# Kernel optimization log

Measured on AMD Instinct MI355X. Metric: run time of the kernel, lower is better.

## Reference

```python
import jax, jax.numpy as jnp
import numpy as np

N_NODES = 50000
N_GRAPHS = 64
HEADS = 4
OUT_CH = 32
HC = HEADS * OUT_CH  # 128
F_IN = 32
EDGE_DIM = 1
NEG_SLOPE = 0.2


def gat_conv(x, edge_index, W, att_src, att_dst, bias, edge_attr=None, W_edge=None, att_edge=None):
    """PyG GATConv (concat=True, add_self_loops=True, fill_value='mean', eval mode)."""
    N = x.shape[0]
    H, C = att_src.shape
    xs = (x @ W).reshape(N, H, C)                      # [N,H,C]
    a_src = (xs * att_src).sum(-1)                     # [N,H]
    a_dst = (xs * att_dst).sum(-1)                     # [N,H]

    src, dst = edge_index[0], edge_index[1]
    loops = jnp.arange(N)
    src_sl = jnp.concatenate([src, loops])
    dst_sl = jnp.concatenate([dst, loops])

    alpha = a_src[src_sl] + a_dst[dst_sl]              # [E+N,H]
    if edge_attr is not None:
        # self-loop edge_attr = per-dst mean of incoming edge_attr (fill_value='mean')
        cnt = jax.ops.segment_sum(jnp.ones_like(dst, dtype=edge_attr.dtype), dst, N)
        loop_attr = jax.ops.segment_sum(edge_attr, dst, N) / jnp.maximum(cnt, 1.0)[:, None]
        ea = jnp.concatenate([edge_attr, loop_attr], axis=0)
        e = (ea @ W_edge).reshape(-1, H, C)
        alpha = alpha + (e * att_edge).sum(-1)

    alpha = jax.nn.leaky_relu(alpha, NEG_SLOPE)
    # segment softmax over incoming edges of each dst node
    amax = jax.ops.segment_max(alpha, dst_sl, N)       # every node has a self loop
    alpha = jnp.exp(alpha - amax[dst_sl])
    denom = jax.ops.segment_sum(alpha, dst_sl, N)
    alpha = alpha / (denom[dst_sl] + 1e-16)

    msg = xs[src_sl] * alpha[:, :, None]               # [E+N,H,C]
    out = jax.ops.segment_sum(msg, dst_sl, N)          # [N,H,C]
    return out.reshape(N, H * C) + bias


def setup_inputs() -> dict:
    key = jax.random.key(0)
    ks = iter(jax.random.split(key, 40))
    d = {}
    d["x"] = jax.random.normal(next(ks), (N_NODES, F_IN), jnp.float32)
    d["covalent_index"] = jax.random.randint(next(ks), (2, 150000), 0, N_NODES)
    d["distance_index"] = jax.random.randint(next(ks), (2, 1600000), 0, N_NODES)
    d["distance_attr"] = jax.random.uniform(next(ks), (1600000, EDGE_DIM), jnp.float32)
    d["batch"] = jnp.sort(jax.random.randint(next(ks), (N_NODES,), 0, N_GRAPHS))

    def p(shape):
        return jax.random.normal(next(ks), shape, jnp.float32) * 0.1

    for name, fin in [("c1", F_IN), ("c2", HC), ("d1", F_IN), ("d2", HC)]:
        d[f"W_{name}"] = p((fin, HC))
        d[f"as_{name}"] = p((HEADS, OUT_CH))
        d[f"ad_{name}"] = p((HEADS, OUT_CH))
        d[f"b_{name}"] = p((HC,))
    for name in ("d1", "d2"):
        d[f"We_{name}"] = p((EDGE_DIM, HC))
        d[f"ae_{name}"] = p((HEADS, OUT_CH))
    d["ff_W"] = p((HC, 128))
    d["ff_b"] = p((128,))
    d["out_W"] = p((128, 1))
    d["out_b"] = p((1,))
    return d


def reference(x, covalent_index, distance_index, distance_attr, batch,
              W_c1, as_c1, ad_c1, b_c1, W_c2, as_c2, ad_c2, b_c2,
              W_d1, as_d1, ad_d1, b_d1, We_d1, ae_d1,
              W_d2, as_d2, ad_d2, b_d2, We_d2, ae_d2,
              ff_W, ff_b, out_W, out_b):
    # covalent branch
    x1 = gat_conv(x, covalent_index, W_c1, as_c1, ad_c1, b_c1)
    x1 = jax.nn.relu(x1)
    x1 = gat_conv(x1, covalent_index, W_c2, as_c2, ad_c2, b_c2)
    # distance branch (with edge attributes)
    x2 = gat_conv(x, distance_index, W_d1, as_d1, ad_d1, b_d1, distance_attr, We_d1, ae_d1)
    x2 = jax.nn.relu(x2)
    x2 = gat_conv(x2, distance_index, W_d2, as_d2, ad_d2, b_d2, distance_attr, We_d2, ae_d2)
    h = (x1 + x2) * 0.5
    # global mean pool per graph
    sums = jax.ops.segment_sum(h, batch, N_GRAPHS)
    cnts = jax.ops.segment_sum(jnp.ones((h.shape[0],), h.dtype), batch, N_GRAPHS)
    g = sums / jnp.maximum(cnts, 1.0)[:, None]
    g = jax.nn.relu(g @ ff_W + ff_b)
    # dropout(p=0.3) treated as identity (eval / deterministic reference)
    return jax.nn.sigmoid(g @ out_W + out_b)
```

## Files before the change

### kernel.cpp

```cpp
#include <hip/hip_runtime.h>
#include <math.h>

#define NEG_SLOPE 0.2f

__device__ __forceinline__ float lrelu(float x){ return x > 0.f ? x : NEG_SLOPE * x; }
__device__ __forceinline__ float bf_lo(unsigned u){ return __uint_as_float(u << 16); }
__device__ __forceinline__ float bf_hi(unsigned u){ return __uint_as_float(u & 0xffff0000u); }
__device__ __forceinline__ unsigned short f2bf(float v){
  unsigned ub = __float_as_uint(v);
  return (unsigned short)((ub + 0x7FFFu + ((ub >> 16) & 1u)) >> 16);
}

template<int K>
__global__ __launch_bounds__(256) void transform2_kernel(
    const float* __restrict__ A, const float* __restrict__ W,
    const float* __restrict__ att_s, const float* __restrict__ att_d,
    unsigned short* __restrict__ xs, float* __restrict__ a_src,
    float* __restrict__ a_dst, int N){
  constexpr int KC = (K < 32) ? K : 32;
  __shared__ float sW[KC][128];
  __shared__ float sA[32][K];
  const int tid = threadIdx.x;
  const int j4  = (tid & 31) * 4;
  const int ng  = tid >> 5;
  const int h   = (tid & 31) >> 3;

  const float4 as = *reinterpret_cast<const float4*>(att_s + j4);
  const float4 ad = *reinterpret_cast<const float4*>(att_d + j4);

  const int ntiles = (N + 31) >> 5;
  for (int tile = blockIdx.x; tile < ntiles; tile += gridDim.x){
    const int n0 = tile << 5;
    for (int idx = tid; idx < 32 * K; idx += 256){
      int nn = idx / K, kk = idx - nn * K;
      int node = n0 + nn;
      sA[nn][kk] = (node < N) ? A[(size_t)node * K + kk] : 0.f;
    }

    float acc[4][4];
    #pragma unroll
    for (int m = 0; m < 4; ++m)
      #pragma unroll
      for (int e = 0; e < 4; ++e) acc[m][e] = 0.f;

    for (int kc0 = 0; kc0 < K; kc0 += KC){
      __syncthreads();
      for (int idx = tid; idx < KC * 128; idx += 256)
        sW[idx >> 7][idx & 127] = W[(size_t)(kc0 + (idx >> 7)) * 128 + (idx & 127)];
      __syncthreads();
      #pragma unroll 4
      for (int k = 0; k < KC; ++k){
        const float4 w = *reinterpret_cast<const float4*>(&sW[k][j4]);
        #pragma unroll
        for (int m = 0; m < 4; ++m){
          const float a = sA[ng * 4 + m][kc0 + k];
          acc[m][0] += a * w.x; acc[m][1] += a * w.y;
          acc[m][2] += a * w.z; acc[m][3] += a * w.w;
        }
      }
    }

    #pragma unroll
    for (int m = 0; m < 4; ++m){
      const int node = n0 + ng * 4 + m;
      const bool ok = node < N;
      if (ok){
        uint2 pk;
        pk.x = (unsigned)f2bf(acc[m][0]) | ((unsigned)f2bf(acc[m][1]) << 16);
        pk.y = (unsigned)f2bf(acc[m][2]) | ((unsigned)f2bf(acc[m][3]) << 16);
        *reinterpret_cast<uint2*>(xs + (size_t)node * 128 + j4) = pk;
      }
      float ss = acc[m][0]*as.x + acc[m][1]*as.y + acc[m][2]*as.z + acc[m][3]*as.w;
      float sd = acc[m][0]*ad.x + acc[m][1]*ad.y + acc[m][2]*ad.z + acc[m][3]*ad.w;
      #pragma unroll
      for (int d = 1; d < 8; d <<= 1){ ss += __shfl_xor(ss, d); sd += __shfl_xor(sd, d); }
      if (ok && (tid & 7) == 0){
        a_src[node * 4 + h] = ss;
        a_dst[node * 4 + h] = sd;
      }
    }
    __syncthreads();
  }
}

__global__ void count_kernel(const int* __restrict__ ei, int E, int* __restrict__ cnt){
  int e = blockIdx.x * blockDim.x + threadIdx.x;
  if (e < E) atomicAdd(&cnt[ei[E + e]], 1);
}

__global__ void blocksum_kernel(const int* __restrict__ cnt, int N, int* __restrict__ bsum){
  const int base = blockIdx.x * 1024;
  int s = 0;
  for (int i = threadIdx.x; i < 1024; i += 256){
    int idx = base + i;
    if (idx < N) s += cnt[idx];
  }
  #pragma unroll
  for (int d = 1; d < 64; d <<= 1) s += __shfl_xor(s, d);
  __shared__ int ws[4];
  if ((threadIdx.x & 63) == 0) ws[threadIdx.x >> 6] = s;
  __syncthreads();
  if (threadIdx.x == 0) bsum[blockIdx.x] = ws[0] + ws[1] + ws[2] + ws[3];
}

__global__ void bscan_kernel(int* __restrict__ bsum, int nb){
  int t = threadIdx.x;
  int v = (t < nb) ? bsum[t] : 0;
  int x = v;
  #pragma unroll
  for (int d = 1; d < 64; d <<= 1){ int y = __shfl_up(x, d); if (t >= d) x += y; }
  if (t < nb) bsum[t] = x - v;
}

__global__ void scanwrite_kernel(const int* __restrict__ cnt, const int* __restrict__ bsum,
                                 int N, int* __restrict__ rp, int* __restrict__ cur){
  const int b = blockIdx.x, t = threadIdx.x;
  const int base = b * 1024 + t * 4;
  int v0=0,v1=0,v2=0,v3=0;
  if (base + 0 < N) v0 = cnt[base + 0];
  if (base + 1 < N) v1 = cnt[base + 1];
  if (base + 2 < N) v2 = cnt[base + 2];
  if (base + 3 < N) v3 = cnt[base + 3];
  const int tsum = v0 + v1 + v2 + v3;
  int x = tsum;
  const int lane = t & 63;
  #pragma unroll
  for (int d = 1; d < 64; d <<= 1){ int y = __shfl_up(x, d); if (lane >= d) x += y; }
  __shared__ int ws[4];
  if (lane == 63) ws[t >> 6] = x;
  __syncthreads();
  int ofs = bsum[b];
  for (int w = 0; w < (t >> 6); ++w) ofs += ws[w];
  int start = ofs + (x - tsum);
  int r1 = start + v0, r2 = r1 + v1, r3 = r2 + v2, r4 = r3 + v3;
  if (base + 0 < N){ rp[base + 1] = r1; cur[base + 0] = start; }
  if (base + 1 < N){ rp[base + 2] = r2; cur[base + 1] = r1; }
  if (base + 2 < N){ rp[base + 3] = r3; cur[base + 2] = r2; }
  if (base + 3 < N){ rp[base + 4] = r4; cur[base + 3] = r3; }
  if (b == 0 && t == 0) rp[0] = 0;
}

__global__ void fill_cov_kernel(const int* __restrict__ ei, int E,
                                int* __restrict__ cur, int* __restrict__ csrc){
  int e = blockIdx.x * blockDim.x + threadIdx.x;
  if (e >= E) return;
  int src = ei[e];
  int dst = ei[E + e];
  int pos = atomicAdd(&cur[dst], 1);
  csrc[pos] = src;
}

__global__ void fill_dist_kernel(const int* __restrict__ ei, const float* __restrict__ eattr,
                                 int E, int* __restrict__ cur, int2* __restrict__ pke){
  int e = blockIdx.x * blockDim.x + threadIdx.x;
  if (e >= E) return;
  int src = ei[e];
  int dst = ei[E + e];
  float ea = eattr[e];
  int pos = atomicAdd(&cur[dst], 1);
  pke[pos] = make_int2(src, __float_as_int(ea));
}

__global__ void loopea_kernel(const int* __restrict__ rp, const int2* __restrict__ pke,
                              float* __restrict__ lea, int N){
  int n = blockIdx.x * blockDim.x + threadIdx.x;
  if (n >= N) return;
  int b = rp[n], e = rp[n+1];
  float s = 0.f;
  for (int i = b; i < e; ++i) s += __int_as_float(pke[i].y);
  lea[n] = s / fmaxf((float)(e - b), 1.f);
}

__global__ void coef_kernel(const float* __restrict__ We1, const float* __restrict__ ae1,
                            const float* __restrict__ We2, const float* __restrict__ ae2,
                            float* __restrict__ coef){
  int t = threadIdx.x;
  if (t < 4){
    float s = 0.f;
    for (int c = 0; c < 32; ++c) s += We1[t*32 + c] * ae1[t*32 + c];
    coef[t] = s;
  } else if (t < 8){
    int h = t - 4;
    float s = 0.f;
    for (int c = 0; c < 32; ++c) s += We2[h*32 + c] * ae2[h*32 + c];
    coef[4 + h] = s;
  }
}

template<bool HASE, bool RELU>
__global__ void gat_kernel(const int* __restrict__ rp, const int* __restrict__ csrc,
                           const int2* __restrict__ pke, const float* __restrict__ loopea,
                           const float* __restrict__ coef,
                           const unsigned short* __restrict__ xs, const float* __restrict__ a_src,
                           const float* __restrict__ a_dst, const float* __restrict__ bias,
                           float* __restrict__ out, int N){
  __shared__ float p_sh[4][64][4];
  __shared__ int   s_sh[4][64];
  const int wv = threadIdx.x >> 6;
  const int lane = threadIdx.x & 63;
  const int n = blockIdx.x * 4 + wv;
  if (n >= N) return;

  const int beg = rp[n], end = rp[n+1];
  const int c = lane * 2;
  const int h = lane >> 4;

  const float4 adv = *reinterpret_cast<const float4*>(a_dst + (size_t)n*4);
  float4 cf = make_float4(0.f,0.f,0.f,0.f);
  if (HASE) cf = *reinterpret_cast<const float4*>(coef);
  const float adh = (h==0)?adv.x:(h==1)?adv.y:(h==2)?adv.z:adv.w;
  const float chh = (h==0)?cf.x:(h==1)?cf.y:(h==2)?cf.z:cf.w;

  float p;
  {
    float lea = HASE ? loopea[n] : 0.f;
    p = __expf(lrelu(a_src[(size_t)n*4 + h] + adh + lea * chh));
  }
  float denom = p;
  unsigned us = *reinterpret_cast<const unsigned*>(xs + (size_t)n*128 + c);
  float accx = p * bf_lo(us);
  float accy = p * bf_hi(us);

  for (int c0 = beg; c0 < end; c0 += 64){
    const int cnt = min(64, end - c0);
    if (lane < cnt){
      int s; float ea = 0.f;
      if (HASE){
        int2 rec = pke[c0 + lane];
        s = rec.x; ea = __int_as_float(rec.y);
      } else {
        s = csrc[c0 + lane];
      }
      const float4 av = *reinterpret_cast<const float4*>(a_src + (size_t)s*4);
      float4 pv;
      pv.x = __expf(lrelu(av.x + adv.x + ea*cf.x));
      pv.y = __expf(lrelu(av.y + adv.y + ea*cf.y));
      pv.z = __expf(lrelu(av.z + adv.z + ea*cf.z));
      pv.w = __expf(lrelu(av.w + adv.w + ea*cf.w));
      *reinterpret_cast<float4*>(&p_sh[wv][lane][0]) = pv;
      s_sh[wv][lane] = s;
    }
    #pragma unroll 4
    for (int i = 0; i < cnt; ++i){
      const int s = s_sh[wv][i];
      const float pf = p_sh[wv][i][h];
      denom += pf;
      unsigned u = *reinterpret_cast<const unsigned*>(xs + (size_t)s*128 + c);
      accx += pf * bf_lo(u);
      accy += pf * bf_hi(u);
    }
  }

  const float inv = 1.f / (denom + 1e-16f);
  float ox = accx * inv + bias[c];
  float oy = accy * inv + bias[c+1];
  if (RELU){ ox = fmaxf(ox, 0.f); oy = fmaxf(oy, 0.f); }
  out[(size_t)n*128 + c]     = ox;
  out[(size_t)n*128 + c + 1] = oy;
}

template<bool COUNT>
__global__ void pool_kernel(const float* __restrict__ a, const int* __restrict__ batch,
                            float* __restrict__ sums, int* __restrict__ cnts, int N){
  const int j = threadIdx.x;
  const int n0 = blockIdx.x * 32;
  const int n1 = min(n0 + 32, N);
  if (n0 >= N) return;
  int g = batch[n0];
  float acc = 0.f;
  int cnt = 0;
  for (int n = n0; n < n1; ++n){
    int gn = batch[n];
    if (gn != g){
      atomicAdd(&sums[g*128 + j], 0.5f * acc);
      if (COUNT && j == 0) atomicAdd(&cnts[g], cnt);
      acc = 0.f; cnt = 0; g = gn;
    }
    acc += a[(size_t)n*128 + j];
    ++cnt;
  }
  atomicAdd(&sums[g*128 + j], 0.5f * acc);
  if (COUNT && j == 0) atomicAdd(&cnts[g], cnt);
}

__global__ void head_kernel(const float* __restrict__ sums, const int* __restrict__ cnts,
                            const float* __restrict__ ffW, const float* __restrict__ ffb,
                            const float* __restrict__ outW, const float* __restrict__ outb,
                            float* __restrict__ out){
  int g = blockIdx.x, j = threadIdx.x;
  __shared__ float mean[128];
  __shared__ float red[128];
  float cnt = fmaxf((float)cnts[g], 1.f);
  mean[j] = sums[g*128 + j] / cnt;
  __syncthreads();
  float acc = ffb[j];
  #pragma unroll 8
  for (int k = 0; k < 128; ++k) acc += mean[k] * ffW[k*128 + j];
  acc = fmaxf(acc, 0.f);
  red[j] = acc * outW[j];
  __syncthreads();
  for (int s = 64; s > 0; s >>= 1){
    if (j < s) red[j] += red[j + s];
    __syncthreads();
  }
  if (j == 0) out[g] = 1.f / (1.f + expf(-(red[0] + outb[0])));
}

extern "C" void kernel_launch(void* const* d_in, const int* in_sizes, int n_in,
                              void* d_out, int out_size, void* d_ws, size_t ws_size,
                              hipStream_t stream) {
  const float* x     = (const float*)d_in[0];
  const int*   cov   = (const int*)d_in[1];
  const int*   dist  = (const int*)d_in[2];
  const float* dattr = (const float*)d_in[3];
  const int*   batch = (const int*)d_in[4];
  const float* W_c1 = (const float*)d_in[5],  *as_c1 = (const float*)d_in[6],
             *ad_c1 = (const float*)d_in[7],  *b_c1  = (const float*)d_in[8];
  const float* W_c2 = (const float*)d_in[9],  *as_c2 = (const float*)d_in[10],
             *ad_c2 = (const float*)d_in[11], *b_c2  = (const float*)d_in[12];
  const float* W_d1 = (const float*)d_in[13], *as_d1 = (const float*)d_in[14],
             *ad_d1 = (const float*)d_in[15], *b_d1  = (const float*)d_in[16];
  const float* W_d2 = (const float*)d_in[17], *as_d2 = (const float*)d_in[18],
             *ad_d2 = (const float*)d_in[19], *b_d2  = (const float*)d_in[20];
  const float* We_d1 = (const float*)d_in[21], *ae_d1 = (const float*)d_in[22];
  const float* We_d2 = (const float*)d_in[23], *ae_d2 = (const float*)d_in[24];
  const float* ffW = (const float*)d_in[25], *ffb = (const float*)d_in[26];
  const float* outW = (const float*)d_in[27], *outb = (const float*)d_in[28];
  float* out = (float*)d_out;

  const int N  = in_sizes[0] / 32;
  const int Ec = in_sizes[1] / 2;
  const int Ed = in_sizes[2] / 2;

  char* p = (char*)d_ws;
  auto alloc = [&](size_t bytes) -> void* {
    void* r = (void*)p;
    p += (bytes + 255) & ~(size_t)255;
    return r;
  };
  float*          act    = (float*)alloc((size_t)N * 128 * 4);
  unsigned short* xs     = (unsigned short*)alloc((size_t)N * 128 * 2);
  float*          a_s    = (float*)alloc((size_t)N * 4 * 4);
  float*          a_d    = (float*)alloc((size_t)N * 4 * 4);
  int*            rp_c   = (int*)alloc((size_t)(N + 1) * 4);
  int*            rp_d   = (int*)alloc((size_t)(N + 1) * 4);
  int*            csrc_c = (int*)alloc((size_t)Ec * 4);
  int2*           pke_d  = (int2*)alloc((size_t)Ed * 8);
  int*            cnt    = (int*)alloc((size_t)N * 4);
  int*            cur    = (int*)alloc((size_t)N * 4);
  float*          lea    = (float*)alloc((size_t)N * 4);
  float*          coef   = (float*)alloc(8 * 4);
  float*          sums   = (float*)alloc(64 * 128 * 4);
  int*            cnts   = (int*)alloc(64 * 4);
  int*            bsum   = (int*)alloc(256 * 4);

  const int TB = 256;
  const int nb = (N + 1023) / 1024;
  hipMemsetAsync(cnt, 0, (size_t)N * 4, stream);
  count_kernel<<<(Ec + TB - 1) / TB, TB, 0, stream>>>(cov, Ec, cnt);
  blocksum_kernel<<<nb, 256, 0, stream>>>(cnt, N, bsum);
  bscan_kernel<<<1, 64, 0, stream>>>(bsum, nb);
  scanwrite_kernel<<<nb, 256, 0, stream>>>(cnt, bsum, N, rp_c, cur);
  fill_cov_kernel<<<(Ec + TB - 1) / TB, TB, 0, stream>>>(cov, Ec, cur, csrc_c);
  hipMemsetAsync(cnt, 0, (size_t)N * 4, stream);
  count_kernel<<<(Ed + TB - 1) / TB, TB, 0, stream>>>(dist, Ed, cnt);
  blocksum_kernel<<<nb, 256, 0, stream>>>(cnt, N, bsum);
  bscan_kernel<<<1, 64, 0, stream>>>(bsum, nb);
  scanwrite_kernel<<<nb, 256, 0, stream>>>(cnt, bsum, N, rp_d, cur);
  fill_dist_kernel<<<(Ed + TB - 1) / TB, TB, 0, stream>>>(dist, dattr, Ed, cur, pke_d);
  loopea_kernel<<<(N + TB - 1) / TB, TB, 0, stream>>>(rp_d, pke_d, lea, N);
  coef_kernel<<<1, 64, 0, stream>>>(We_d1, ae_d1, We_d2, ae_d2, coef);

  hipMemsetAsync(sums, 0, 64 * 128 * 4, stream);
  hipMemsetAsync(cnts, 0, 64 * 4, stream);

  const int gatGrid  = (N + 3) / 4;
  const int poolGrid = (N + 31) / 32;
  const int TFB = 1024;
  transform2_kernel<32><<<TFB, 256, 0, stream>>>(x, W_c1, as_c1, ad_c1, xs, a_s, a_d, N);
  gat_kernel<false, true><<<gatGrid, 256, 0, stream>>>(rp_c, csrc_c, nullptr, nullptr, nullptr,
                                                       xs, a_s, a_d, b_c1, act, N);
  transform2_kernel<128><<<TFB, 256, 0, stream>>>(act, W_c2, as_c2, ad_c2, xs, a_s, a_d, N);
  gat_kernel<false, false><<<gatGrid, 256, 0, stream>>>(rp_c, csrc_c, nullptr, nullptr, nullptr,
                                                        xs, a_s, a_d, b_c2, act, N);
  pool_kernel<true><<<poolGrid, 128, 0, stream>>>(act, batch, sums, cnts, N);
  transform2_kernel<32><<<TFB, 256, 0, stream>>>(x, W_d1, as_d1, ad_d1, xs, a_s, a_d, N);
  gat_kernel<true, true><<<gatGrid, 256, 0, stream>>>(rp_d, nullptr, pke_d, lea, coef,
                                                      xs, a_s, a_d, b_d1, act, N);
  transform2_kernel<128><<<TFB, 256, 0, stream>>>(act, W_d2, as_d2, ad_d2, xs, a_s, a_d, N);
  gat_kernel<true, false><<<gatGrid, 256, 0, stream>>>(rp_d, nullptr, pke_d, lea, coef + 4,
                                                       xs, a_s, a_d, b_d2, act, N);
  pool_kernel<false><<<poolGrid, 128, 0, stream>>>(act, batch, sums, nullptr, N);
  head_kernel<<<64, 128, 0, stream>>>(sums, cnts, ffW, ffb, outW, outb, out);
}
```

Baseline: 673.5 us.

## Two-pass bucketed CSR fill for distance edges to localize scatter writes

Replaces the single-pass per-destination atomic scatter of distance edges with a two-pass scheme. Edges are first bucketed into groups of 64 destinations using one atomic per bucket, then each bucket is sorted locally with shared-memory atomics. This is meant to reduce global atomic contention and the cost of randomly scattered writes, in exchange for an extra pass over a temporary buffer. Packing src into 16 bits breaks correctness when N exceeds 65536; N is 50000 here, so it holds. bcur is sized for at most 1024 buckets.

```diff
diff --git a/kernel.cpp b/kernel.cpp
--- a/kernel.cpp
+++ b/kernel.cpp
@@ -150,15 +150,43 @@
   csrc[pos] = src;
 }
 
-__global__ void fill_dist_kernel(const int* __restrict__ ei, const float* __restrict__ eattr,
-                                 int E, int* __restrict__ cur, int2* __restrict__ pke){
+__global__ void bcurinit_kernel(const int* __restrict__ rp, int* __restrict__ bcur,
+                                int N, int nbuk){
+  int b = blockIdx.x * blockDim.x + threadIdx.x;
+  if (b < nbuk) bcur[b] = rp[min(b << 6, N)];
+}
+
+__global__ void bucket_kernel(const int* __restrict__ ei, const float* __restrict__ eattr,
+                              int E, int* __restrict__ bcur, int2* __restrict__ tmp){
   int e = blockIdx.x * blockDim.x + threadIdx.x;
   if (e >= E) return;
   int src = ei[e];
   int dst = ei[E + e];
   float ea = eattr[e];
-  int pos = atomicAdd(&cur[dst], 1);
-  pke[pos] = make_int2(src, __float_as_int(ea));
+  int pos = atomicAdd(&bcur[dst >> 6], 1);
+  tmp[pos] = make_int2(src | ((dst & 63) << 16), __float_as_int(ea));
+}
+
+__global__ void fill_dist2_kernel(const int* __restrict__ rp, int N,
+                                  const int2* __restrict__ tmp, int2* __restrict__ pke){
+  __shared__ int lcnt[64];
+  __shared__ int lrp[64];
+  const int b = blockIdx.x;
+  const int t = (int)threadIdx.x;
+  const int d0 = b << 6;
+  if (t < 64){
+    lcnt[t] = 0;
+    lrp[t] = rp[min(d0 + t, N)];
+  }
+  __syncthreads();
+  const int wb = lrp[0];
+  const int we = rp[min(d0 + 64, N)];
+  for (int i = wb + t; i < we; i += (int)blockDim.x){
+    int2 rec = tmp[i];
+    int d = (rec.x >> 16) & 63;
+    int rank = atomicAdd(&lcnt[d], 1);
+    pke[lrp[d] + rank] = make_int2(rec.x & 0xffff, rec.y);
+  }
 }
 
 __global__ void loopea_kernel(const int* __restrict__ rp, const int2* __restrict__ pke,
@@ -346,6 +374,7 @@
   int*            rp_d   = (int*)alloc((size_t)(N + 1) * 4);
   int*            csrc_c = (int*)alloc((size_t)Ec * 4);
   int2*           pke_d  = (int2*)alloc((size_t)Ed * 8);
+  int2*           tmp_d  = (int2*)alloc((size_t)Ed * 8);
   int*            cnt    = (int*)alloc((size_t)N * 4);
   int*            cur    = (int*)alloc((size_t)N * 4);
   float*          lea    = (float*)alloc((size_t)N * 4);
@@ -353,9 +382,11 @@
   float*          sums   = (float*)alloc(64 * 128 * 4);
   int*            cnts   = (int*)alloc(64 * 4);
   int*            bsum   = (int*)alloc(256 * 4);
+  int*            bcur   = (int*)alloc(1024 * 4);
 
   const int TB = 256;
-  const int nb = (N + 1023) / 1024;
+  const int nb   = (N + 1023) / 1024;
+  const int nbuk = (N + 63) / 64;
   hipMemsetAsync(cnt, 0, (size_t)N * 4, stream);
   count_kernel<<<(Ec + TB - 1) / TB, TB, 0, stream>>>(cov, Ec, cnt);
   blocksum_kernel<<<nb, 256, 0, stream>>>(cnt, N, bsum);
@@ -367,7 +398,9 @@
   blocksum_kernel<<<nb, 256, 0, stream>>>(cnt, N, bsum);
   bscan_kernel<<<1, 64, 0, stream>>>(bsum, nb);
   scanwrite_kernel<<<nb, 256, 0, stream>>>(cnt, bsum, N, rp_d, cur);
-  fill_dist_kernel<<<(Ed + TB - 1) / TB, TB, 0, stream>>>(dist, dattr, Ed, cur, pke_d);
+  bcurinit_kernel<<<(nbuk + 255) / 256, 256, 0, stream>>>(rp_d, bcur, N, nbuk);
+  bucket_kernel<<<(Ed + TB - 1) / TB, TB, 0, stream>>>(dist, dattr, Ed, bcur, tmp_d);
+  fill_dist2_kernel<<<nbuk, 256, 0, stream>>>(rp_d, N, tmp_d, pke_d);
   loopea_kernel<<<(N + TB - 1) / TB, TB, 0, stream>>>(rp_d, pke_d, lea, N);
   coef_kernel<<<1, 64, 0, stream>>>(We_d1, ae_d1, We_d2, ae_d2, coef);
 
```

Result: slower. 948.6 us (+40.8%).
